# Optimization experiments

Hardware: AMD Instinct MI355X
Metric: run time of the kernel (lower is better)

Reference implementation:

```python
import jax, jax.numpy as jnp
import numpy as np

EPS = np.float32(np.finfo(float).eps)  # 2.220446049250313e-16, matches torch code
TOP_K = 2


def setup_inputs() -> dict:
    key = jax.random.key(0)
    ks = jax.random.split(key, 7)
    B, D, H, E = 8192, 1024, 4096, 8
    # init scales mirror the torch MLP init (std = sqrt(2/(m+n)), sqrt(1/m))
    return {
        "inp": jax.random.normal(ks[0], (B, D), dtype=jnp.float32),
        "gate_w": jax.random.normal(ks[1], (E, D), dtype=jnp.float32) * np.sqrt(1.0 / D).astype(np.float32),
        "gate_b": jax.random.normal(ks[2], (E,), dtype=jnp.float32) * 0.01,
        "W1": jax.random.normal(ks[3], (E, H, D), dtype=jnp.float32) * np.sqrt(2.0 / (H + D)).astype(np.float32),
        "b1": jax.random.normal(ks[4], (E, H), dtype=jnp.float32) * np.sqrt(1.0 / H).astype(np.float32),
        "W2": jax.random.normal(ks[5], (E, D, H), dtype=jnp.float32) * np.sqrt(2.0 / (D + H)).astype(np.float32),
        "b2": jax.random.normal(ks[6], (E, D), dtype=jnp.float32) * np.sqrt(1.0 / D).astype(np.float32),
    }


def _moe_forward(inp, gate_w, gate_b, W1, b1, W2, b2):
    B = inp.shape[0]
    E = gate_w.shape[0]
    # --- NaiveGate: linear -> top-k -> softmax -> scatter into dense gates ---
    logits = inp @ gate_w.T + gate_b                      # [B, E]
    top_vals, top_idx = jax.lax.top_k(logits, TOP_K)      # [B, k]
    top_gates = jax.nn.softmax(top_vals, axis=-1)         # top_k > 1 branch
    gates = jnp.zeros((B, E), dtype=jnp.float32)
    gates = gates.at[jnp.arange(B)[:, None], top_idx].set(top_gates)

    # --- Experts: 2-layer MLP, ReLU after every linear (sigmoid_layer=-1) ---
    h = jax.nn.relu(jnp.einsum('bd,ehd->ebh', inp, W1) + b1[:, None, :])   # [E, B, H]
    out = jax.nn.relu(jnp.einsum('ebh,edh->ebd', h, W2) + b2[:, None, :])  # [E, B, D]

    # --- SparseDispatcher.combine: exp -> gate-weighted scatter-sum -> +eps -> log ---
    # Dense-equivalent: gates are exactly zero for non-routed (token, expert)
    # pairs, so the weighted sum matches the sparse scatter exactly.
    combined = jnp.einsum('be,ebd->bd', gates, jnp.exp(out))
    return jnp.log(combined + EPS)


def reference(inp, gate_w, gate_b, W1, b1, W2, b2):
    return _moe_forward(inp, gate_w, gate_b, W1, b1, W2, b2)
```

## Files before the change

### kernel.cpp

```cpp
#include <hip/hip_runtime.h>
#include <hip/hip_bf16.h>
#include <math.h>

#define B_TOK 8192
#define DDIM  1024
#define HDIM  4096
#define NEXP  8
#define CAP   17408

typedef unsigned short u16;
using f32x4  = __attribute__((ext_vector_type(4))) float;
using bf16x8 = __attribute__((ext_vector_type(8))) short;

__device__ __forceinline__ u16 f2bf(float f) {
  union { float f; unsigned u; } v; v.f = f;
  unsigned r = v.u + 0x7FFFu + ((v.u >> 16) & 1u);
  return (u16)(r >> 16);
}

__device__ __forceinline__ void load_lds16(const void* g, void* l) {
  __builtin_amdgcn_global_load_lds((const __attribute__((address_space(1))) void*)g,
                                   (__attribute__((address_space(3))) void*)l,
                                   16, 0, 0);
}

__global__ __launch_bounds__(256) void cvtw_kernel(const float4* __restrict__ w1,
                                                   const float4* __restrict__ w2,
                                                   ushort4* __restrict__ w1b,
                                                   ushort4* __restrict__ w2b, int n4each) {
  for (int i = blockIdx.x * 256 + threadIdx.x; i < 2 * n4each; i += gridDim.x * 256) {
    const float4* src = (i < n4each) ? w1 : w2;
    ushort4*      dst = (i < n4each) ? w1b : w2b;
    int j = (i < n4each) ? i : i - n4each;
    float4 v = src[j];
    ushort4 o;
    o.x = f2bf(v.x); o.y = f2bf(v.y); o.z = f2bf(v.z); o.w = f2bf(v.w);
    dst[j] = o;
  }
}

__global__ __launch_bounds__(256) void gate_kernel(
    const float* __restrict__ inp, const float* __restrict__ gw,
    const float* __restrict__ gb, int* __restrict__ tok_e,
    float* __restrict__ tok_g, int* __restrict__ counts,
    ushort4* __restrict__ Xb4)
{
  int gtid = blockIdx.x * 256 + threadIdx.x;
  int tok  = gtid >> 6;
  int lane = threadIdx.x & 63;
  if (tok >= B_TOK) return;
  const float4* X = (const float4*)(inp + (size_t)tok * DDIM);
  float4 x[4];
#pragma unroll
  for (int j = 0; j < 4; ++j) x[j] = X[j * 64 + lane];
  ushort4* Xrow = Xb4 + (size_t)tok * (DDIM / 4);
#pragma unroll
  for (int j = 0; j < 4; ++j) {
    ushort4 o;
    o.x = f2bf(x[j].x); o.y = f2bf(x[j].y); o.z = f2bf(x[j].z); o.w = f2bf(x[j].w);
    Xrow[j * 64 + lane] = o;
  }
  float lg[NEXP];
#pragma unroll
  for (int e = 0; e < NEXP; ++e) {
    const float4* W = (const float4*)(gw + e * DDIM);
    double s = 0.0;
#pragma unroll
    for (int j = 0; j < 4; ++j) {
      float4 w = W[j * 64 + lane];
      s += (double)x[j].x * w.x + (double)x[j].y * w.y
         + (double)x[j].z * w.z + (double)x[j].w * w.w;
    }
#pragma unroll
    for (int o = 32; o > 0; o >>= 1) s += __shfl_xor(s, o);
    lg[e] = (float)(s + (double)gb[e]);
  }
  if (lane == 0) {
    int i0 = 0; float v0 = lg[0];
#pragma unroll
    for (int e = 1; e < NEXP; ++e) if (lg[e] > v0) { v0 = lg[e]; i0 = e; }
    int i1 = -1; float v1 = -3.4e38f;
#pragma unroll
    for (int e = 0; e < NEXP; ++e) if (e != i0 && lg[e] > v1) { v1 = lg[e]; i1 = e; }
    float t   = __expf(v1 - v0);
    float inv = 1.0f / (1.0f + t);
    tok_e[2 * tok] = i0; tok_e[2 * tok + 1] = i1;
    tok_g[2 * tok] = inv; tok_g[2 * tok + 1] = t * inv;
    atomicAdd(&counts[i0], 1);
    atomicAdd(&counts[i1], 1);
  }
}

__global__ __launch_bounds__(256) void scatter_kernel(
    const int* __restrict__ tok_e, const float* __restrict__ tok_g,
    const int* __restrict__ counts, int* __restrict__ cursors,
    int* __restrict__ slot_token, float* __restrict__ slot_gate,
    int* __restrict__ offs, int* __restrict__ padded)
{
  __shared__ int soffs[NEXP];
  if (threadIdx.x == 0) {
    int off = 0;
    for (int e = 0; e < NEXP; ++e) {
      soffs[e] = off;
      int p = (counts[e] + 127) & ~127;
      off += p;
      if (blockIdx.x == 0) { offs[e] = soffs[e]; padded[e] = p; }
    }
  }
  __syncthreads();
  int b = blockIdx.x * 256 + threadIdx.x;
  if (b >= B_TOK) return;
#pragma unroll
  for (int k = 0; k < 2; ++k) {
    int e   = tok_e[2 * b + k];
    float g = tok_g[2 * b + k];
    int pos = atomicAdd(&cursors[e], 1);
    int s   = soffs[e] + pos;
    slot_token[s] = b;
    slot_gate[s]  = g;
  }
}


#define STAGE(kt_) do {                                                   \
    _Pragma("unroll") for (int g = 0; g < 4; ++g) {                       \
      load_lds16(pAg[g] + (kt_) * 64, &As[(g * 256 + tid) * 8]);           \
      load_lds16(pBg[g] + (kt_) * 64, &Bs[(g * 256 + tid) * 8]);           \
    } } while (0)

#define GEMM_BODY(NT_) do {                                               \
    const int NT = (NT_);                                                 \
    _Pragma("unroll 1")                                                   \
    for (int t = 0; t < NT; ++t) {                                        \
      STAGE(t);                                                           \
      __syncthreads();                                                    \
      bf16x8 af[4][2], bfr[4][2];                                         \
      _Pragma("unroll") for (int m = 0; m < 4; ++m)                       \
        _Pragma("unroll") for (int kk = 0; kk < 2; ++kk)                  \
          af[m][kk] = *(const bf16x8*)&As[(wm + m*16 + fr)*64             \
                                        + (((kk*4 + fq) ^ fr7) * 8)];     \
      _Pragma("unroll") for (int n = 0; n < 4; ++n)                       \
        _Pragma("unroll") for (int kk = 0; kk < 2; ++kk)                  \
          bfr[n][kk] = *(const bf16x8*)&Bs[(wn + n*16 + fr)*64            \
                                        + (((kk*4 + fq) ^ fr7) * 8)];     \
      _Pragma("unroll") for (int kk = 0; kk < 2; ++kk)                    \
      _Pragma("unroll") for (int m = 0; m < 4; ++m)                       \
      _Pragma("unroll") for (int n = 0; n < 4; ++n)                       \
        acc[m][n] = __builtin_amdgcn_mfma_f32_16x16x32_bf16(              \
            af[m][kk], bfr[n][kk], acc[m][n], 0, 0, 0);                   \
      __syncthreads();                                                    \
    } } while (0)

__global__ __launch_bounds__(256, 4) void gemm1_kernel(
    const u16* __restrict__ Xb, const u16* __restrict__ W1b,
    const float* __restrict__ b1, const int* __restrict__ slot_token,
    const int* __restrict__ offs, const int* __restrict__ padded,
    u16* __restrict__ Hb)
{
  const int h   = blockIdx.x + 32 * (blockIdx.y + 64 * blockIdx.z);
  const int e   = h & 7;
  const int r   = h >> 3;
  const int mi  = r >> 5;
  const int nti = r & 31;
  if (mi * 128 >= padded[e]) return;
  const int base_slot = offs[e] + mi * 128;
  const int n0 = nti * 128;

  __shared__ __align__(16) u16 As[8192];
  __shared__ __align__(16) u16 Bs[8192];
  __shared__ int toks[128];

  const int tid = threadIdx.x;
  if (tid < 128) toks[tid] = slot_token[base_slot + tid];
  __syncthreads();

  const u16* pAg[4];
  const u16* pBg[4];
#pragma unroll
  for (int g = 0; g < 4; ++g) {
    int i = g * 256 + tid, rr = i >> 3, sl = i & 7;
    int kc = (sl ^ (rr & 7)) * 8;
    pAg[g] = Xb + (size_t)toks[rr] * DDIM + kc;
    pBg[g] = W1b + ((size_t)e * HDIM + (size_t)(n0 + rr)) * DDIM + kc;
  }

  const int wave = tid >> 6, lane = tid & 63;
  const int wm = (wave >> 1) * 64, wn = (wave & 1) * 64;
  const int fr = lane & 15, fq = lane >> 4, fr7 = fr & 7;

  f32x4 acc[4][4];
#pragma unroll
  for (int m = 0; m < 4; ++m)
#pragma unroll
    for (int n = 0; n < 4; ++n) acc[m][n] = f32x4{0.f, 0.f, 0.f, 0.f};

  GEMM_BODY(DDIM / 64);

#pragma unroll
  for (int n = 0; n < 4; ++n) {
    int col = n0 + wn + n * 16 + fr;
    float bias = b1[e * HDIM + col];
#pragma unroll
    for (int m = 0; m < 4; ++m) {
      int row0 = wm + m * 16 + fq * 4;
#pragma unroll
      for (int j = 0; j < 4; ++j) {
        float v = acc[m][n][j] + bias;
        v = v > 0.f ? v : 0.f;
        Hb[(size_t)(base_slot + row0 + j) * HDIM + col] = f2bf(v);
      }
    }
  }
}

__global__ __launch_bounds__(256, 4) void gemm2_kernel(
    const u16* __restrict__ Hb, const u16* __restrict__ W2b,
    const float* __restrict__ b2, const float* __restrict__ slot_gate,
    const int* __restrict__ slot_token, const int* __restrict__ offs,
    const int* __restrict__ padded, float* __restrict__ out)
{
  const int h   = blockIdx.x + 8 * (blockIdx.y + 64 * blockIdx.z);
  const int e   = h & 7;
  const int r   = h >> 3;
  const int mi  = r >> 3;
  const int nti = r & 7;
  if (mi * 128 >= padded[e]) return;
  const int base_slot = offs[e] + mi * 128;
  const int n0 = nti * 128;

  __shared__ __align__(16) u16 As[8192];
  __shared__ __align__(16) u16 Bs[8192];
  __shared__ int   toks[128];
  __shared__ float gts[128];

  const int tid = threadIdx.x;
  if (tid < 128) {
    toks[tid] = slot_token[base_slot + tid];
    gts[tid]  = slot_gate[base_slot + tid];
  }
  __syncthreads();

  const u16* pAg[4];
  const u16* pBg[4];
#pragma unroll
  for (int g = 0; g < 4; ++g) {
    int i = g * 256 + tid, rr = i >> 3, sl = i & 7;
    int kc = (sl ^ (rr & 7)) * 8;
    pAg[g] = Hb + (size_t)(base_slot + rr) * HDIM + kc;
    pBg[g] = W2b + ((size_t)e * DDIM + (size_t)(n0 + rr)) * HDIM + kc;
  }

  const int wave = tid >> 6, lane = tid & 63;
  const int wm = (wave >> 1) * 64, wn = (wave & 1) * 64;
  const int fr = lane & 15, fq = lane >> 4, fr7 = fr & 7;

  f32x4 acc[4][4];
#pragma unroll
  for (int m = 0; m < 4; ++m)
#pragma unroll
    for (int n = 0; n < 4; ++n) acc[m][n] = f32x4{0.f, 0.f, 0.f, 0.f};

  GEMM_BODY(HDIM / 64);

#pragma unroll
  for (int n = 0; n < 4; ++n) {
    int col = n0 + wn + n * 16 + fr;
    float bias = b2[e * DDIM + col];
#pragma unroll
    for (int m = 0; m < 4; ++m) {
      int row0 = wm + m * 16 + fq * 4;
#pragma unroll
      for (int j = 0; j < 4; ++j) {
        int row = row0 + j;
        float v = acc[m][n][j] + bias;
        v = v > 0.f ? v : 0.f;
        float p = gts[row] * __expf(v);
        atomicAdd(&out[(size_t)toks[row] * DDIM + col], p);
      }
    }
  }
}

__global__ __launch_bounds__(256) void log_kernel(float4* __restrict__ out, int n4) {
  const float EPS = 2.220446049250313e-16f;
  for (int i = blockIdx.x * 256 + threadIdx.x; i < n4; i += gridDim.x * 256) {
    float4 v = out[i];
    v.x = logf(v.x + EPS);
    v.y = logf(v.y + EPS);
    v.z = logf(v.z + EPS);
    v.w = logf(v.w + EPS);
    out[i] = v;
  }
}

extern "C" void kernel_launch(void* const* d_in, const int* in_sizes, int n_in,
                              void* d_out, int out_size, void* d_ws, size_t ws_size,
                              hipStream_t stream)
{
  const float* inp = (const float*)d_in[0];
  const float* gw  = (const float*)d_in[1];
  const float* gb  = (const float*)d_in[2];
  const float* W1  = (const float*)d_in[3];
  const float* b1  = (const float*)d_in[4];
  const float* W2  = (const float*)d_in[5];
  const float* b2  = (const float*)d_in[6];
  float* out = (float*)d_out;

  char* ws = (char*)d_ws;
  size_t off = 0;
  auto alloc = [&](size_t bytes) {
    void* p = ws + off;
    off = (off + bytes + 255) & ~(size_t)255;
    return p;
  };
  u16*   Xb  = (u16*)alloc((size_t)B_TOK * DDIM * 2);
  u16*   W1b = (u16*)alloc((size_t)NEXP * HDIM * DDIM * 2);
  u16*   W2b = (u16*)alloc((size_t)NEXP * DDIM * HDIM * 2);
  u16*   Hb  = (u16*)alloc((size_t)CAP * HDIM * 2);
  int*   slot_token = (int*)alloc(CAP * 4);
  float* slot_gate  = (float*)alloc(CAP * 4);
  int*   tok_e = (int*)alloc(B_TOK * 2 * 4);
  float* tok_g = (float*)alloc(B_TOK * 2 * 4);
  int*   counts  = (int*)alloc(32);
  int*   offs    = (int*)alloc(32);
  int*   padded  = (int*)alloc(32);
  int*   cursors = (int*)alloc(32);

  (void)hipMemsetAsync(counts, 0, 32, stream);
  (void)hipMemsetAsync(cursors, 0, 32, stream);
  (void)hipMemsetAsync(slot_token, 0, CAP * 4, stream);
  (void)hipMemsetAsync(slot_gate, 0, CAP * 4, stream);
  (void)hipMemsetAsync(out, 0, (size_t)out_size * 4, stream);

  gate_kernel<<<B_TOK / 4, 256, 0, stream>>>(inp, gw, gb, tok_e, tok_g, counts,
                                             (ushort4*)Xb);
  cvtw_kernel<<<4096, 256, 0, stream>>>((const float4*)W1, (const float4*)W2,
                                        (ushort4*)W1b, (ushort4*)W2b,
                                        NEXP * HDIM * DDIM / 4);
  scatter_kernel<<<B_TOK / 256, 256, 0, stream>>>(tok_e, tok_g, counts, cursors,
                                                  slot_token, slot_gate, offs, padded);

  gemm1_kernel<<<dim3(32, 64, NEXP), 256, 0, stream>>>(
      Xb, W1b, b1, slot_token, offs, padded, Hb);
  gemm2_kernel<<<dim3(8, 64, NEXP), 256, 0, stream>>>(
      Hb, W2b, b2, slot_gate, slot_token, offs, padded, out);

  log_kernel<<<2048, 256, 0, stream>>>((float4*)out, out_size / 4);
}
```

Before: 771.9 us.

## Replace atomic scatter-add combine with per-slot stores and gather combine kernel

New measurement: 723.5 us. 1.07x faster.

```diff
diff --git a/kernel.cpp b/kernel.cpp
--- a/kernel.cpp
+++ b/kernel.cpp
@@ -95,6 +95,7 @@
     const int* __restrict__ tok_e, const float* __restrict__ tok_g,
     const int* __restrict__ counts, int* __restrict__ cursors,
     int* __restrict__ slot_token, float* __restrict__ slot_gate,
+    int* __restrict__ tok_slot,
     int* __restrict__ offs, int* __restrict__ padded)
 {
   __shared__ int soffs[NEXP];
@@ -118,6 +119,7 @@
     int s   = soffs[e] + pos;
     slot_token[s] = b;
     slot_gate[s]  = g;
+    tok_slot[2 * b + k] = s;
   }
 }
 
@@ -216,8 +218,8 @@
 __global__ __launch_bounds__(256, 4) void gemm2_kernel(
     const u16* __restrict__ Hb, const u16* __restrict__ W2b,
     const float* __restrict__ b2, const float* __restrict__ slot_gate,
-    const int* __restrict__ slot_token, const int* __restrict__ offs,
-    const int* __restrict__ padded, float* __restrict__ out)
+    const int* __restrict__ offs, const int* __restrict__ padded,
+    float* __restrict__ P)
 {
   const int h   = blockIdx.x + 8 * (blockIdx.y + 64 * blockIdx.z);
   const int e   = h & 7;
@@ -230,14 +232,10 @@
 
   __shared__ __align__(16) u16 As[8192];
   __shared__ __align__(16) u16 Bs[8192];
-  __shared__ int   toks[128];
   __shared__ float gts[128];
 
   const int tid = threadIdx.x;
-  if (tid < 128) {
-    toks[tid] = slot_token[base_slot + tid];
-    gts[tid]  = slot_gate[base_slot + tid];
-  }
+  if (tid < 128) gts[tid] = slot_gate[base_slot + tid];
   __syncthreads();
 
   const u16* pAg[4];
@@ -274,22 +272,29 @@
         int row = row0 + j;
         float v = acc[m][n][j] + bias;
         v = v > 0.f ? v : 0.f;
-        float p = gts[row] * __expf(v);
-        atomicAdd(&out[(size_t)toks[row] * DDIM + col], p);
+        P[(size_t)(base_slot + row) * DDIM + col] = gts[row] * __expf(v);
       }
     }
   }
 }
 
-__global__ __launch_bounds__(256) void log_kernel(float4* __restrict__ out, int n4) {
+__global__ __launch_bounds__(256) void combine_kernel(
+    const float4* __restrict__ P4, const int* __restrict__ tok_slot,
+    float4* __restrict__ out4)
+{
   const float EPS = 2.220446049250313e-16f;
-  for (int i = blockIdx.x * 256 + threadIdx.x; i < n4; i += gridDim.x * 256) {
-    float4 v = out[i];
-    v.x = logf(v.x + EPS);
-    v.y = logf(v.y + EPS);
-    v.z = logf(v.z + EPS);
-    v.w = logf(v.w + EPS);
-    out[i] = v;
+  const int total = B_TOK * (DDIM / 4);
+  for (int i = blockIdx.x * 256 + threadIdx.x; i < total; i += gridDim.x * 256) {
+    int tok = i >> 8, d4 = i & 255;
+    int s0 = tok_slot[2 * tok], s1 = tok_slot[2 * tok + 1];
+    float4 a = P4[(size_t)s0 * (DDIM / 4) + d4];
+    float4 b = P4[(size_t)s1 * (DDIM / 4) + d4];
+    float4 v;
+    v.x = logf(a.x + b.x + EPS);
+    v.y = logf(a.y + b.y + EPS);
+    v.z = logf(a.z + b.z + EPS);
+    v.w = logf(a.w + b.w + EPS);
+    out4[i] = v;
   }
 }
 
@@ -315,22 +320,21 @@
   };
   u16*   Xb  = (u16*)alloc((size_t)B_TOK * DDIM * 2);
   u16*   W1b = (u16*)alloc((size_t)NEXP * HDIM * DDIM * 2);
+  float* P   = (float*)Xb;
   u16*   W2b = (u16*)alloc((size_t)NEXP * DDIM * HDIM * 2);
   u16*   Hb  = (u16*)alloc((size_t)CAP * HDIM * 2);
   int*   slot_token = (int*)alloc(CAP * 4);
   float* slot_gate  = (float*)alloc(CAP * 4);
-  int*   tok_e = (int*)alloc(B_TOK * 2 * 4);
-  float* tok_g = (float*)alloc(B_TOK * 2 * 4);
+  int*   tok_e    = (int*)alloc(B_TOK * 2 * 4);
+  float* tok_g    = (float*)alloc(B_TOK * 2 * 4);
+  int*   tok_slot = (int*)alloc(B_TOK * 2 * 4);
   int*   counts  = (int*)alloc(32);
+  int*   cursors = (int*)alloc(32);
   int*   offs    = (int*)alloc(32);
   int*   padded  = (int*)alloc(32);
-  int*   cursors = (int*)alloc(32);
-
-  (void)hipMemsetAsync(counts, 0, 32, stream);
-  (void)hipMemsetAsync(cursors, 0, 32, stream);
-  (void)hipMemsetAsync(slot_token, 0, CAP * 4, stream);
-  (void)hipMemsetAsync(slot_gate, 0, CAP * 4, stream);
-  (void)hipMemsetAsync(out, 0, (size_t)out_size * 4, stream);
+
+  (void)hipMemsetAsync(counts, 0, 288, stream);
+  (void)hipMemsetAsync(slot_token, 0, (size_t)CAP * 8, stream);
 
   gate_kernel<<<B_TOK / 4, 256, 0, stream>>>(inp, gw, gb, tok_e, tok_g, counts,
                                              (ushort4*)Xb);
@@ -338,12 +342,13 @@
                                         (ushort4*)W1b, (ushort4*)W2b,
                                         NEXP * HDIM * DDIM / 4);
   scatter_kernel<<<B_TOK / 256, 256, 0, stream>>>(tok_e, tok_g, counts, cursors,
-                                                  slot_token, slot_gate, offs, padded);
+                                                  slot_token, slot_gate, tok_slot,
+                                                  offs, padded);
 
   gemm1_kernel<<<dim3(32, 64, NEXP), 256, 0, stream>>>(
       Xb, W1b, b1, slot_token, offs, padded, Hb);
   gemm2_kernel<<<dim3(8, 64, NEXP), 256, 0, stream>>>(
-      Hb, W2b, b2, slot_gate, slot_token, offs, padded, out);
-
-  log_kernel<<<2048, 256, 0, stream>>>((float4*)out, out_size / 4);
-}
+      Hb, W2b, b2, slot_gate, offs, padded, P);
+
+  combine_kernel<<<2048, 256, 0, stream>>>((const float4*)P, tok_slot, (float4*)out);
+}
```
